# Performance work log

Hardware: AMD Instinct MI355X
Metric: run time of the kernel (lower is better)

## Reference

```python
import jax, jax.numpy as jnp
import numpy as np

N_NODES = 50000
N_EDGES = 600000
IN_DIM = 128
HID = 256
OUT = 3


def setup_inputs() -> dict:
    key = jax.random.key(0)
    ks = jax.random.split(key, 10)
    x = jax.random.normal(ks[0], (N_NODES, IN_DIM), dtype=jnp.float32)
    edge_index = jax.random.randint(ks[1], (2, N_EDGES), 0, N_NODES, dtype=jnp.int64)
    s = lambda k, shp: jax.random.normal(k, shp, dtype=jnp.float32) * (1.0 / np.sqrt(shp[0]))
    return {
        "x": x,
        "edge_index": edge_index,
        # SAGEConv1: lin_l (applied to aggregated neighbors, with bias), lin_r (root, no bias)
        "W1l": s(ks[2], (IN_DIM, HID)), "b1": jnp.zeros((HID,), jnp.float32), "W1r": s(ks[3], (IN_DIM, HID)),
        # SAGEConv2
        "W2l": s(ks[4], (HID, HID)), "b2": jnp.zeros((HID,), jnp.float32), "W2r": s(ks[5], (HID, HID)),
        # classification head
        "Wh": s(ks[6], (HID, OUT)), "bh": jnp.zeros((OUT,), jnp.float32),
    }


def _sage_conv(x, edge_index, Wl, b, Wr):
    """PyG SAGEConv with mean aggregation: out = lin_l(mean_{j->i} x_j) + lin_r(x_i)."""
    src, dst = edge_index[0], edge_index[1]
    n = x.shape[0]
    # gather source features and scatter-mean onto targets
    msg_sum = jax.ops.segment_sum(x[src], dst, num_segments=n)          # [N, d]
    deg = jax.ops.segment_sum(jnp.ones((src.shape[0],), x.dtype), dst, num_segments=n)
    mean = msg_sum / jnp.maximum(deg, 1.0)[:, None]                      # isolated nodes -> 0
    return mean @ Wl + b + x @ Wr


def reference(x, edge_index, W1l, b1, W1r, W2l, b2, W2r, Wh, bh):
    h = jax.nn.relu(_sage_conv(x, edge_index, W1l, b1, W1r))
    # dropout(p=0.2) is identity in eval mode
    h = jax.nn.relu(_sage_conv(h, edge_index, W2l, b2, W2r))
    return h @ Wh + bh
```

## Files before the change

### kernel.cpp

```cpp
#include <hip/hip_runtime.h>
#include <hip/hip_bf16.h>

#define N_NODES 50000
#define N_EDGES 600000
#define IN_DIM 128
#define HID 256
#define OUT_DIM 3

#define M_PAD 50048

#define SCAN_B 256
#define SCAN_NB ((N_NODES + SCAN_B - 1) / SCAN_B)

typedef __bf16 bf16x8 __attribute__((ext_vector_type(8)));
typedef float f32x4 __attribute__((ext_vector_type(4)));

static __device__ __forceinline__ unsigned short f2b(float f) {
    union { float f; unsigned u; } u; u.f = f;
    unsigned r = u.u + 0x7fffu + ((u.u >> 16) & 1u);
    return (unsigned short)(r >> 16);
}
static __device__ __forceinline__ float b2f(unsigned short b) {
    union { unsigned u; float f; } u; u.u = ((unsigned)b) << 16;
    return u.f;
}

static __device__ __forceinline__ void gload16(const void* g, unsigned short* l) {
    __builtin_amdgcn_global_load_lds((const __attribute__((address_space(1))) void*)g,
                                     (__attribute__((address_space(3))) void*)l, 16, 0, 0);
}


__global__ void count_deg_kernel(const int* __restrict__ dst, int* __restrict__ counts) {
    int e = blockIdx.x * blockDim.x + threadIdx.x;
    if (e < N_EDGES) atomicAdd(&counts[dst[e]], 1);
}

__global__ __launch_bounds__(256) void block_sum_kernel(const int* __restrict__ counts,
                                                        int* __restrict__ partial) {
    int node = blockIdx.x * SCAN_B + threadIdx.x;
    int v = (node < N_NODES) ? counts[node] : 0;
#pragma unroll
    for (int off = 32; off > 0; off >>= 1) v += __shfl_down(v, off);
    __shared__ int ws[4];
    if ((threadIdx.x & 63) == 0) ws[threadIdx.x >> 6] = v;
    __syncthreads();
    if (threadIdx.x == 0) partial[blockIdx.x] = ws[0] + ws[1] + ws[2] + ws[3];
}

__global__ __launch_bounds__(256) void scan_partial_kernel(int* __restrict__ partial) {
    __shared__ int s[SCAN_B];
    int t = threadIdx.x;
    int v = (t < SCAN_NB) ? partial[t] : 0;
    s[t] = v;
    __syncthreads();
    for (int off = 1; off < SCAN_B; off <<= 1) {
        int u = (t >= off) ? s[t - off] : 0;
        __syncthreads();
        s[t] += u;
        __syncthreads();
    }
    if (t < SCAN_NB) partial[t] = s[t] - v;
}

__global__ __launch_bounds__(256) void write_rowptr_kernel(const int* __restrict__ counts,
                                                           const int* __restrict__ partial,
                                                           int* __restrict__ row_ptr) {
    __shared__ int s[SCAN_B];
    int t = threadIdx.x;
    int node = blockIdx.x * SCAN_B + t;
    int v = (node < N_NODES) ? counts[node] : 0;
    s[t] = v;
    __syncthreads();
    for (int off = 1; off < SCAN_B; off <<= 1) {
        int u = (t >= off) ? s[t - off] : 0;
        __syncthreads();
        s[t] += u;
        __syncthreads();
    }
    if (node < N_NODES) row_ptr[node] = partial[blockIdx.x] + s[t] - v;
    if (node == 0) row_ptr[N_NODES] = N_EDGES;
}

__global__ void fill_csr_kernel(const int* __restrict__ src, const int* __restrict__ dst,
                                const int* __restrict__ row_ptr, int* __restrict__ cursor,
                                int* __restrict__ csr_src) {
    int e = blockIdx.x * blockDim.x + threadIdx.x;
    if (e < N_EDGES) {
        int d = dst[e];
        int pos = atomicAdd(&cursor[d], 1);
        csr_src[row_ptr[d] + pos] = src[e];
    }
}


__global__ void cast_f2b_kernel(const float* __restrict__ in, unsigned short* __restrict__ out, int n) {
    int i = blockIdx.x * blockDim.x + threadIdx.x;
    if (i * 4 < n) {
        float4 v = ((const float4*)in)[i];
        ushort4 o;
        o.x = f2b(v.x); o.y = f2b(v.y); o.z = f2b(v.z); o.w = f2b(v.w);
        ((ushort4*)out)[i] = o;
    }
}

__global__ void tcast4_kernel(const float* __restrict__ W1l, const float* __restrict__ W1r,
                              const float* __restrict__ W2l, const float* __restrict__ W2r,
                              unsigned short* __restrict__ W1lt, unsigned short* __restrict__ W1rt,
                              unsigned short* __restrict__ W2lt, unsigned short* __restrict__ W2rt) {
    int i = blockIdx.x * blockDim.x + threadIdx.x;
    const float* in; unsigned short* out; int K, base;
    if (i < 32768)        { in = W1l; out = W1lt; K = IN_DIM; base = 0; }
    else if (i < 65536)   { in = W1r; out = W1rt; K = IN_DIM; base = 32768; }
    else if (i < 131072)  { in = W2l; out = W2lt; K = HID;    base = 65536; }
    else if (i < 196608)  { in = W2r; out = W2rt; K = HID;    base = 131072; }
    else return;
    int j = i - base;
    int k = j >> 8;
    int n = j & 255;
    out[(size_t)n * K + k] = f2b(in[j]);
}

__global__ void init_out_kernel(const float* __restrict__ bh, float* __restrict__ out) {
    int i = blockIdx.x * blockDim.x + threadIdx.x;
    if (i < N_NODES * 3) out[i] = bh[i % 3];
}


static __device__ __forceinline__ void addv(float* acc, uint4 v) {
    acc[0] += b2f((unsigned short)(v.x & 0xffff));
    acc[1] += b2f((unsigned short)(v.x >> 16));
    acc[2] += b2f((unsigned short)(v.y & 0xffff));
    acc[3] += b2f((unsigned short)(v.y >> 16));
    acc[4] += b2f((unsigned short)(v.z & 0xffff));
    acc[5] += b2f((unsigned short)(v.z >> 16));
    acc[6] += b2f((unsigned short)(v.w & 0xffff));
    acc[7] += b2f((unsigned short)(v.w >> 16));
}

static __device__ __forceinline__ uint4 pack8(const float* a) {
    uint4 pk;
    pk.x = (unsigned)f2b(a[0]) | ((unsigned)f2b(a[1]) << 16);
    pk.y = (unsigned)f2b(a[2]) | ((unsigned)f2b(a[3]) << 16);
    pk.z = (unsigned)f2b(a[4]) | ((unsigned)f2b(a[5]) << 16);
    pk.w = (unsigned)f2b(a[6]) | ((unsigned)f2b(a[7]) << 16);
    return pk;
}

__global__ __launch_bounds__(256) void agg_mean256_kernel(const unsigned short* __restrict__ feat,
                                                          const int* __restrict__ row_ptr,
                                                          const int* __restrict__ csr_src,
                                                          unsigned short* __restrict__ out) {
    int node = blockIdx.x * 4 + (threadIdx.x >> 6);
    if (node >= N_NODES) return;
    int lane = threadIdx.x & 63;
    int half = lane >> 5, lh = lane & 31;
    const uint4* f4 = (const uint4*)feat;
    float acc[8];
#pragma unroll
    for (int j = 0; j < 8; j++) acc[j] = 0.f;
    int beg = row_ptr[node], end = row_ptr[node + 1];
    int i = beg;
    for (; i + 4 <= end; i += 4) {
        int sA = csr_src[i + half];
        int sB = csr_src[i + 2 + half];
        uint4 vA = f4[(size_t)sA * 32 + lh];
        uint4 vB = f4[(size_t)sB * 32 + lh];
        addv(acc, vA);
        addv(acc, vB);
    }
    if (i + 2 <= end) {
        int s = csr_src[i + half];
        addv(acc, f4[(size_t)s * 32 + lh]);
        i += 2;
    }
    if (i < end && half == 0) {
        int s = csr_src[i];
        addv(acc, f4[(size_t)s * 32 + lh]);
    }
    float inv = (end > beg) ? 1.0f / (float)(end - beg) : 0.0f;
#pragma unroll
    for (int j = 0; j < 8; j++) {
        acc[j] += __shfl_xor(acc[j], 32);
        acc[j] *= inv;
    }
    if (half == 0) ((uint4*)(out + (size_t)node * 256))[lh] = pack8(acc);
}

__global__ __launch_bounds__(256) void agg_mean128_kernel(const unsigned short* __restrict__ feat,
                                                          const int* __restrict__ row_ptr,
                                                          const int* __restrict__ csr_src,
                                                          unsigned short* __restrict__ out) {
    int node = blockIdx.x * 4 + (threadIdx.x >> 6);
    if (node >= N_NODES) return;
    int lane = threadIdx.x & 63;
    int q = lane >> 4, lq = lane & 15;
    const uint4* f4 = (const uint4*)feat;
    float acc[8];
#pragma unroll
    for (int j = 0; j < 8; j++) acc[j] = 0.f;
    int beg = row_ptr[node], end = row_ptr[node + 1];
    int i = beg;
    for (; i + 8 <= end; i += 8) {
        int sA = csr_src[i + q];
        int sB = csr_src[i + 4 + q];
        uint4 vA = f4[(size_t)sA * 16 + lq];
        uint4 vB = f4[(size_t)sB * 16 + lq];
        addv(acc, vA);
        addv(acc, vB);
    }
    if (i + 4 <= end) {
        int s = csr_src[i + q];
        addv(acc, f4[(size_t)s * 16 + lq]);
        i += 4;
    }
    int rem = end - i;
    if (q < rem) {
        int s = csr_src[i + q];
        addv(acc, f4[(size_t)s * 16 + lq]);
    }
    float inv = (end > beg) ? 1.0f / (float)(end - beg) : 0.0f;
#pragma unroll
    for (int j = 0; j < 8; j++) {
        acc[j] += __shfl_xor(acc[j], 32);
        acc[j] += __shfl_xor(acc[j], 16);
        acc[j] *= inv;
    }
    if (q == 0) ((uint4*)(out + (size_t)node * 128))[lq] = pack8(acc);
}


#define GEMM_STAGE_AND_MFMA(A, Wt)                                                          \
    for (int k0 = 0; k0 < K; k0 += 64) {                                                    \
        __syncthreads();                                                                    \
        _Pragma("unroll")                                                                   \
        for (int r = 0; r < 4; r++) {                                                       \
            int kb = skb + 2 * r;                                                           \
            gload16(A + (size_t)(m0 + sm) * K + k0 + kb * 8, &As[kb * 1024 + sm * 8]);      \
            gload16(Wt + (size_t)(n0 + sm) * K + k0 + kb * 8, &Bs[kb * 1024 + sm * 8]);     \
        }                                                                                   \
        __syncthreads();                                                                    \
        _Pragma("unroll")                                                                   \
        for (int kk = 0; kk < 2; kk++) {                                                    \
            int kbb = kk * 4 + quad;                                                        \
            bf16x8 a[2], b[8];                                                              \
            a[0] = *(const bf16x8*)&As[kbb * 1024 + (w * 32 + lr) * 8];                     \
            a[1] = *(const bf16x8*)&As[kbb * 1024 + (w * 32 + 16 + lr) * 8];                \
            _Pragma("unroll")                                                               \
            for (int nt = 0; nt < 8; nt++)                                                  \
                b[nt] = *(const bf16x8*)&Bs[kbb * 1024 + (nt * 16 + lr) * 8];               \
            _Pragma("unroll")                                                               \
            for (int mt = 0; mt < 2; mt++)                                                  \
                _Pragma("unroll")                                                           \
                for (int nt = 0; nt < 8; nt++)                                              \
                    acc[mt][nt] = __builtin_amdgcn_mfma_f32_16x16x32_bf16(a[mt], b[nt],     \
                                                                          acc[mt][nt], 0, 0, 0); \
        }                                                                                   \
    }

__global__ __launch_bounds__(256) void gemm_mfma_kernel(
    const unsigned short* __restrict__ A0, const unsigned short* __restrict__ W0t,
    const unsigned short* __restrict__ A1, const unsigned short* __restrict__ W1t,
    const float* __restrict__ bias, unsigned short* __restrict__ out,
    int M, int K) {
    __shared__ __align__(16) unsigned short As[8 * 128 * 8];
    __shared__ __align__(16) unsigned short Bs[8 * 128 * 8];

    const int t = threadIdx.x;
    const int w = t >> 6, l = t & 63;
    const int quad = l >> 4, lr = l & 15;
    const int m0 = blockIdx.x * 128, n0 = blockIdx.y * 128;
    const int sm = t & 127, skb = t >> 7;

    f32x4 acc[2][8];
    const f32x4 zero = {0.f, 0.f, 0.f, 0.f};
#pragma unroll
    for (int mt = 0; mt < 2; mt++)
#pragma unroll
        for (int nt = 0; nt < 8; nt++) acc[mt][nt] = zero;

    float bias_r[8];
#pragma unroll
    for (int nt = 0; nt < 8; nt++) bias_r[nt] = bias[n0 + nt * 16 + lr];

    GEMM_STAGE_AND_MFMA(A0, W0t)
    GEMM_STAGE_AND_MFMA(A1, W1t)

#pragma unroll
    for (int mt = 0; mt < 2; mt++)
#pragma unroll
        for (int r = 0; r < 4; r++) {
            int gm = m0 + w * 32 + mt * 16 + quad * 4 + r;
            if (gm >= M) continue;
            unsigned short* orow = out + (size_t)gm * HID;
#pragma unroll
            for (int nt = 0; nt < 8; nt++) {
                float v = fmaxf(acc[mt][nt][r] + bias_r[nt], 0.f);
                orow[n0 + nt * 16 + lr] = f2b(v);
            }
        }
}

__global__ __launch_bounds__(256) void gemm_mfma_head_kernel(
    const unsigned short* __restrict__ A0, const unsigned short* __restrict__ W0t,
    const unsigned short* __restrict__ A1, const unsigned short* __restrict__ W1t,
    const float* __restrict__ bias, const float* __restrict__ Wh,
    float* __restrict__ out, int M, int K) {
    __shared__ __align__(16) unsigned short As[8 * 128 * 8];
    __shared__ __align__(16) unsigned short Bs[8 * 128 * 8];

    const int t = threadIdx.x;
    const int w = t >> 6, l = t & 63;
    const int quad = l >> 4, lr = l & 15;
    const int m0 = blockIdx.x * 128, n0 = blockIdx.y * 128;
    const int sm = t & 127, skb = t >> 7;

    f32x4 acc[2][8];
    const f32x4 zero = {0.f, 0.f, 0.f, 0.f};
#pragma unroll
    for (int mt = 0; mt < 2; mt++)
#pragma unroll
        for (int nt = 0; nt < 8; nt++) acc[mt][nt] = zero;

    float bias_r[8];
    float wh_r[8][3];
#pragma unroll
    for (int nt = 0; nt < 8; nt++) {
        int gn = n0 + nt * 16 + lr;
        bias_r[nt] = bias[gn];
        wh_r[nt][0] = Wh[gn * 3 + 0];
        wh_r[nt][1] = Wh[gn * 3 + 1];
        wh_r[nt][2] = Wh[gn * 3 + 2];
    }

    GEMM_STAGE_AND_MFMA(A0, W0t)
    GEMM_STAGE_AND_MFMA(A1, W1t)

#pragma unroll
    for (int mt = 0; mt < 2; mt++)
#pragma unroll
        for (int r = 0; r < 4; r++) {
            int gm = m0 + w * 32 + mt * 16 + quad * 4 + r;
            float p0 = 0.f, p1 = 0.f, p2 = 0.f;
#pragma unroll
            for (int nt = 0; nt < 8; nt++) {
                float v = fmaxf(acc[mt][nt][r] + bias_r[nt], 0.f);
                p0 += v * wh_r[nt][0];
                p1 += v * wh_r[nt][1];
                p2 += v * wh_r[nt][2];
            }
#pragma unroll
            for (int off = 1; off < 16; off <<= 1) {
                p0 += __shfl_xor(p0, off);
                p1 += __shfl_xor(p1, off);
                p2 += __shfl_xor(p2, off);
            }
            if (lr == 0 && gm < M) {
                atomicAdd(&out[(size_t)gm * 3 + 0], p0);
                atomicAdd(&out[(size_t)gm * 3 + 1], p1);
                atomicAdd(&out[(size_t)gm * 3 + 2], p2);
            }
        }
}


extern "C" void kernel_launch(void* const* d_in, const int* in_sizes, int n_in,
                              void* d_out, int out_size, void* d_ws, size_t ws_size,
                              hipStream_t stream) {
    const float* x   = (const float*)d_in[0];
    const int*   ei  = (const int*)d_in[1];
    const int*   src = ei;
    const int*   dst = ei + N_EDGES;
    const float* W1l = (const float*)d_in[2];
    const float* b1  = (const float*)d_in[3];
    const float* W1r = (const float*)d_in[4];
    const float* W2l = (const float*)d_in[5];
    const float* b2  = (const float*)d_in[6];
    const float* W2r = (const float*)d_in[7];
    const float* Wh  = (const float*)d_in[8];
    const float* bh  = (const float*)d_in[9];
    float* out = (float*)d_out;

    char* ws = (char*)d_ws;
    size_t off = 0;
    auto alloc = [&](size_t bytes) -> void* {
        void* p = ws + off;
        off = (off + bytes + 255) & ~(size_t)255;
        return p;
    };
    int* counts   = (int*)alloc((size_t)N_NODES * 4);
    int* row_ptr  = (int*)alloc((size_t)(N_NODES + 1) * 4);
    int* cursor   = (int*)alloc((size_t)N_NODES * 4);
    int* partial  = (int*)alloc((size_t)SCAN_NB * 4);
    int* csr_src  = (int*)alloc((size_t)N_EDGES * 4);
    unsigned short* xb   = (unsigned short*)alloc((size_t)M_PAD * IN_DIM * 2);
    unsigned short* agg  = (unsigned short*)alloc((size_t)M_PAD * HID * 2);
    unsigned short* h1   = (unsigned short*)alloc((size_t)M_PAD * HID * 2);
    unsigned short* W1lt = (unsigned short*)alloc((size_t)IN_DIM * HID * 2);
    unsigned short* W1rt = (unsigned short*)alloc((size_t)IN_DIM * HID * 2);
    unsigned short* W2lt = (unsigned short*)alloc((size_t)HID * HID * 2);
    unsigned short* W2rt = (unsigned short*)alloc((size_t)HID * HID * 2);

    hipMemsetAsync(counts, 0, (size_t)N_NODES * 4, stream);
    hipMemsetAsync(cursor, 0, (size_t)N_NODES * 4, stream);

    const int eblocks = (N_EDGES + 255) / 256;
    count_deg_kernel<<<eblocks, 256, 0, stream>>>(dst, counts);
    block_sum_kernel<<<SCAN_NB, SCAN_B, 0, stream>>>(counts, partial);
    scan_partial_kernel<<<1, SCAN_B, 0, stream>>>(partial);
    write_rowptr_kernel<<<SCAN_NB, SCAN_B, 0, stream>>>(counts, partial, row_ptr);
    fill_csr_kernel<<<eblocks, 256, 0, stream>>>(src, dst, row_ptr, cursor, csr_src);

    {
        int n = N_NODES * IN_DIM;
        cast_f2b_kernel<<<(n / 4 + 255) / 256, 256, 0, stream>>>(x, xb, n);
        tcast4_kernel<<<(196608 + 255) / 256, 256, 0, stream>>>(W1l, W1r, W2l, W2r,
                                                                W1lt, W1rt, W2lt, W2rt);
        init_out_kernel<<<(N_NODES * 3 + 255) / 256, 256, 0, stream>>>(bh, out);
    }

    const int nblocks4 = (N_NODES + 3) / 4;
    dim3 gg((N_NODES + 127) / 128, HID / 128);

    agg_mean128_kernel<<<nblocks4, 256, 0, stream>>>(xb, row_ptr, csr_src, agg);
    gemm_mfma_kernel<<<gg, 256, 0, stream>>>(agg, W1lt, xb, W1rt, b1, h1, N_NODES, IN_DIM);

    agg_mean256_kernel<<<nblocks4, 256, 0, stream>>>(h1, row_ptr, csr_src, agg);
    gemm_mfma_head_kernel<<<gg, 256, 0, stream>>>(agg, W2lt, h1, W2rt, b2, Wh, out, N_NODES, HID);
}
```

Baseline: 307.9 us.

## Replace LDS-staged GEMM with direct register-loaded MFMA waves and narrower N tiles

Drops the shared-memory staging (global_load_lds plus barriers) in both GEMM kernels. Each wave now loads its A and W fragments straight from global memory into registers and feeds MFMA, with K as a template parameter so the loop fully unrolls. The N tile shrinks from 128 to 64 and the grid doubles in y, with a 4-blocks-per-SM occupancy hint. This removes LDS traffic and barrier stalls, but A rows are reused across fewer N columns and fragments are fetched repeatedly from global memory, which depends on the caches absorbing the duplication.

```diff
diff --git a/kernel.cpp b/kernel.cpp
--- a/kernel.cpp
+++ b/kernel.cpp
@@ -23,11 +23,6 @@
 static __device__ __forceinline__ float b2f(unsigned short b) {
     union { unsigned u; float f; } u; u.u = ((unsigned)b) << 16;
     return u.f;
-}
-
-static __device__ __forceinline__ void gload16(const void* g, unsigned short* l) {
-    __builtin_amdgcn_global_load_lds((const __attribute__((address_space(1))) void*)g,
-                                     (__attribute__((address_space(3))) void*)l, 16, 0, 0);
 }
 
 
@@ -230,102 +225,92 @@
 }
 
 
-#define GEMM_STAGE_AND_MFMA(A, Wt)                                                          \
-    for (int k0 = 0; k0 < K; k0 += 64) {                                                    \
-        __syncthreads();                                                                    \
-        _Pragma("unroll")                                                                   \
-        for (int r = 0; r < 4; r++) {                                                       \
-            int kb = skb + 2 * r;                                                           \
-            gload16(A + (size_t)(m0 + sm) * K + k0 + kb * 8, &As[kb * 1024 + sm * 8]);      \
-            gload16(Wt + (size_t)(n0 + sm) * K + k0 + kb * 8, &Bs[kb * 1024 + sm * 8]);     \
-        }                                                                                   \
-        __syncthreads();                                                                    \
-        _Pragma("unroll")                                                                   \
-        for (int kk = 0; kk < 2; kk++) {                                                    \
-            int kbb = kk * 4 + quad;                                                        \
-            bf16x8 a[2], b[8];                                                              \
-            a[0] = *(const bf16x8*)&As[kbb * 1024 + (w * 32 + lr) * 8];                     \
-            a[1] = *(const bf16x8*)&As[kbb * 1024 + (w * 32 + 16 + lr) * 8];                \
-            _Pragma("unroll")                                                               \
-            for (int nt = 0; nt < 8; nt++)                                                  \
-                b[nt] = *(const bf16x8*)&Bs[kbb * 1024 + (nt * 16 + lr) * 8];               \
-            _Pragma("unroll")                                                               \
-            for (int mt = 0; mt < 2; mt++)                                                  \
-                _Pragma("unroll")                                                           \
-                for (int nt = 0; nt < 8; nt++)                                              \
-                    acc[mt][nt] = __builtin_amdgcn_mfma_f32_16x16x32_bf16(a[mt], b[nt],     \
-                                                                          acc[mt][nt], 0, 0, 0); \
-        }                                                                                   \
-    }
-
-__global__ __launch_bounds__(256) void gemm_mfma_kernel(
+template <int K>
+static __device__ __forceinline__ void gemm_wave(const unsigned short* __restrict__ A,
+                                                 const unsigned short* __restrict__ Wt,
+                                                 int arow, int n0, int lr, int quad,
+                                                 f32x4 (&acc)[2][4]) {
+#pragma unroll
+    for (int ks = 0; ks < K / 32; ks++) {
+        const int koff = ks * 32 + quad * 8;
+        bf16x8 a[2], b[4];
+#pragma unroll
+        for (int mt = 0; mt < 2; mt++)
+            a[mt] = *(const bf16x8*)(A + (size_t)(arow + mt * 16 + lr) * K + koff);
+#pragma unroll
+        for (int nt = 0; nt < 4; nt++)
+            b[nt] = *(const bf16x8*)(Wt + (size_t)(n0 + nt * 16 + lr) * K + koff);
+#pragma unroll
+        for (int mt = 0; mt < 2; mt++)
+#pragma unroll
+            for (int nt = 0; nt < 4; nt++)
+                acc[mt][nt] = __builtin_amdgcn_mfma_f32_16x16x32_bf16(a[mt], b[nt], acc[mt][nt], 0, 0, 0);
+    }
+}
+
+template <int K>
+__global__ __launch_bounds__(256, 4) void gemm_reg_kernel(
     const unsigned short* __restrict__ A0, const unsigned short* __restrict__ W0t,
     const unsigned short* __restrict__ A1, const unsigned short* __restrict__ W1t,
-    const float* __restrict__ bias, unsigned short* __restrict__ out,
-    int M, int K) {
-    __shared__ __align__(16) unsigned short As[8 * 128 * 8];
-    __shared__ __align__(16) unsigned short Bs[8 * 128 * 8];
-
+    const float* __restrict__ bias, unsigned short* __restrict__ out, int M) {
     const int t = threadIdx.x;
     const int w = t >> 6, l = t & 63;
     const int quad = l >> 4, lr = l & 15;
-    const int m0 = blockIdx.x * 128, n0 = blockIdx.y * 128;
-    const int sm = t & 127, skb = t >> 7;
-
-    f32x4 acc[2][8];
+    const int arow = blockIdx.x * 128 + w * 32;
+    const int n0 = blockIdx.y * 64;
+
+    f32x4 acc[2][4];
     const f32x4 zero = {0.f, 0.f, 0.f, 0.f};
 #pragma unroll
     for (int mt = 0; mt < 2; mt++)
 #pragma unroll
-        for (int nt = 0; nt < 8; nt++) acc[mt][nt] = zero;
-
-    float bias_r[8];
-#pragma unroll
-    for (int nt = 0; nt < 8; nt++) bias_r[nt] = bias[n0 + nt * 16 + lr];
-
-    GEMM_STAGE_AND_MFMA(A0, W0t)
-    GEMM_STAGE_AND_MFMA(A1, W1t)
+        for (int nt = 0; nt < 4; nt++) acc[mt][nt] = zero;
+
+    float bias_r[4];
+#pragma unroll
+    for (int nt = 0; nt < 4; nt++) bias_r[nt] = bias[n0 + nt * 16 + lr];
+
+    gemm_wave<K>(A0, W0t, arow, n0, lr, quad, acc);
+    gemm_wave<K>(A1, W1t, arow, n0, lr, quad, acc);
 
 #pragma unroll
     for (int mt = 0; mt < 2; mt++)
 #pragma unroll
         for (int r = 0; r < 4; r++) {
-            int gm = m0 + w * 32 + mt * 16 + quad * 4 + r;
+            int gm = arow + mt * 16 + quad * 4 + r;
             if (gm >= M) continue;
             unsigned short* orow = out + (size_t)gm * HID;
 #pragma unroll
-            for (int nt = 0; nt < 8; nt++) {
+            for (int nt = 0; nt < 4; nt++) {
                 float v = fmaxf(acc[mt][nt][r] + bias_r[nt], 0.f);
                 orow[n0 + nt * 16 + lr] = f2b(v);
             }
         }
 }
 
-__global__ __launch_bounds__(256) void gemm_mfma_head_kernel(
+template <int K>
+__global__ __launch_bounds__(256, 4) void gemm_reg_head_kernel(
     const unsigned short* __restrict__ A0, const unsigned short* __restrict__ W0t,
     const unsigned short* __restrict__ A1, const unsigned short* __restrict__ W1t,
     const float* __restrict__ bias, const float* __restrict__ Wh,
-    float* __restrict__ out, int M, int K) {
-    __shared__ __align__(16) unsigned short As[8 * 128 * 8];
-    __shared__ __align__(16) unsigned short Bs[8 * 128 * 8];
-
+    float* __restrict__ out, int M) {
     const int t = threadIdx.x;
     const int w = t >> 6, l = t & 63;
     const int quad = l >> 4, lr = l & 15;
-    const int m0 = blockIdx.x * 128, n0 = blockIdx.y * 128;
-    const int sm = t & 127, skb = t >> 7;
-
-    f32x4 acc[2][8];
+    const int arow = blockIdx.x * 128 + w * 32;
+    const int n0 = blockIdx.y * 64;
+
+    f32x4 acc[2][4];
     const f32x4 zero = {0.f, 0.f, 0.f, 0.f};
 #pragma unroll
     for (int mt = 0; mt < 2; mt++)
 #pragma unroll
-        for (int nt = 0; nt < 8; nt++) acc[mt][nt] = zero;
-
-    float bias_r[8];
-    float wh_r[8][3];
-#pragma unroll
-    for (int nt = 0; nt < 8; nt++) {
+        for (int nt = 0; nt < 4; nt++) acc[mt][nt] = zero;
+
+    float bias_r[4];
+    float wh_r[4][3];
+#pragma unroll
+    for (int nt = 0; nt < 4; nt++) {
         int gn = n0 + nt * 16 + lr;
         bias_r[nt] = bias[gn];
         wh_r[nt][0] = Wh[gn * 3 + 0];
@@ -333,17 +318,17 @@
         wh_r[nt][2] = Wh[gn * 3 + 2];
     }
 
-    GEMM_STAGE_AND_MFMA(A0, W0t)
-    GEMM_STAGE_AND_MFMA(A1, W1t)
+    gemm_wave<K>(A0, W0t, arow, n0, lr, quad, acc);
+    gemm_wave<K>(A1, W1t, arow, n0, lr, quad, acc);
 
 #pragma unroll
     for (int mt = 0; mt < 2; mt++)
 #pragma unroll
         for (int r = 0; r < 4; r++) {
-            int gm = m0 + w * 32 + mt * 16 + quad * 4 + r;
+            int gm = arow + mt * 16 + quad * 4 + r;
             float p0 = 0.f, p1 = 0.f, p2 = 0.f;
 #pragma unroll
-            for (int nt = 0; nt < 8; nt++) {
+            for (int nt = 0; nt < 4; nt++) {
                 float v = fmaxf(acc[mt][nt][r] + bias_r[nt], 0.f);
                 p0 += v * wh_r[nt][0];
                 p1 += v * wh_r[nt][1];
@@ -420,11 +405,11 @@
     }
 
     const int nblocks4 = (N_NODES + 3) / 4;
-    dim3 gg((N_NODES + 127) / 128, HID / 128);
+    dim3 gg((N_NODES + 127) / 128, HID / 64);
 
     agg_mean128_kernel<<<nblocks4, 256, 0, stream>>>(xb, row_ptr, csr_src, agg);
-    gemm_mfma_kernel<<<gg, 256, 0, stream>>>(agg, W1lt, xb, W1rt, b1, h1, N_NODES, IN_DIM);
+    gemm_reg_kernel<IN_DIM><<<gg, 256, 0, stream>>>(agg, W1lt, xb, W1rt, b1, h1, N_NODES);
 
     agg_mean256_kernel<<<nblocks4, 256, 0, stream>>>(h1, row_ptr, csr_src, agg);
-    gemm_mfma_head_kernel<<<gg, 256, 0, stream>>>(agg, W2lt, h1, W2rt, b2, Wh, out, N_NODES, HID);
-}
+    gemm_reg_head_kernel<HID><<<gg, 256, 0, stream>>>(agg, W2lt, h1, W2rt, b2, Wh, out, N_NODES);
+}
```

Result: slower. 352.2 us (+14.4%).

## Double-buffer GEMM tiles with register prefetch instead of direct LDS loads

Applied to the files above, without the earlier changes.

Replaces the single-buffer global_load_lds staging in both fused SAGE GEMM kernels with a register-prefetched, double-buffered LDS pipeline over K chunks of 32. The next tile's global loads are issued before the MFMAs on the current buffer, so memory latency can overlap compute and one barrier per iteration is dropped. The K chunk shrinks from 64 to 32, so there are more iterations, and staging through registers adds VGPR pressure and extra LDS write instructions.

```diff
diff --git a/kernel.cpp b/kernel.cpp
--- a/kernel.cpp
+++ b/kernel.cpp
@@ -23,11 +23,6 @@
 static __device__ __forceinline__ float b2f(unsigned short b) {
     union { unsigned u; float f; } u; u.u = ((unsigned)b) << 16;
     return u.f;
-}
-
-static __device__ __forceinline__ void gload16(const void* g, unsigned short* l) {
-    __builtin_amdgcn_global_load_lds((const __attribute__((address_space(1))) void*)g,
-                                     (__attribute__((address_space(3))) void*)l, 16, 0, 0);
 }
 
 
@@ -230,47 +225,77 @@
 }
 
 
-#define GEMM_STAGE_AND_MFMA(A, Wt)                                                          \
-    for (int k0 = 0; k0 < K; k0 += 64) {                                                    \
-        __syncthreads();                                                                    \
-        _Pragma("unroll")                                                                   \
-        for (int r = 0; r < 4; r++) {                                                       \
-            int kb = skb + 2 * r;                                                           \
-            gload16(A + (size_t)(m0 + sm) * K + k0 + kb * 8, &As[kb * 1024 + sm * 8]);      \
-            gload16(Wt + (size_t)(n0 + sm) * K + k0 + kb * 8, &Bs[kb * 1024 + sm * 8]);     \
-        }                                                                                   \
-        __syncthreads();                                                                    \
-        _Pragma("unroll")                                                                   \
-        for (int kk = 0; kk < 2; kk++) {                                                    \
-            int kbb = kk * 4 + quad;                                                        \
-            bf16x8 a[2], b[8];                                                              \
-            a[0] = *(const bf16x8*)&As[kbb * 1024 + (w * 32 + lr) * 8];                     \
-            a[1] = *(const bf16x8*)&As[kbb * 1024 + (w * 32 + 16 + lr) * 8];                \
-            _Pragma("unroll")                                                               \
-            for (int nt = 0; nt < 8; nt++)                                                  \
-                b[nt] = *(const bf16x8*)&Bs[kbb * 1024 + (nt * 16 + lr) * 8];               \
-            _Pragma("unroll")                                                               \
-            for (int mt = 0; mt < 2; mt++)                                                  \
-                _Pragma("unroll")                                                           \
-                for (int nt = 0; nt < 8; nt++)                                              \
-                    acc[mt][nt] = __builtin_amdgcn_mfma_f32_16x16x32_bf16(a[mt], b[nt],     \
-                                                                          acc[mt][nt], 0, 0, 0); \
-        }                                                                                   \
-    }
-
-__global__ __launch_bounds__(256) void gemm_mfma_kernel(
+template <int KP>
+static __device__ __forceinline__ void gemm_pipe_loop(
     const unsigned short* __restrict__ A0, const unsigned short* __restrict__ W0t,
     const unsigned short* __restrict__ A1, const unsigned short* __restrict__ W1t,
-    const float* __restrict__ bias, unsigned short* __restrict__ out,
-    int M, int K) {
-    __shared__ __align__(16) unsigned short As[8 * 128 * 8];
-    __shared__ __align__(16) unsigned short Bs[8 * 128 * 8];
+    unsigned short* As, unsigned short* Bs,
+    int m0, int n0, int t, int w, int quad, int lr, f32x4 (&acc)[2][8]) {
+    constexpr int KI = KP / 32;
+    constexpr int NIT = 2 * KI;
+    const int kb = t & 3;
+    const int r  = t >> 2;
+
+    const unsigned short* Aa[2] = {A0, A1};
+    const unsigned short* Wa[2] = {W0t, W1t};
+
+    uint4 ra0, ra1, rb0, rb1;
+    auto gload = [&](int it) {
+        int p = it / KI;
+        int k0 = (it % KI) * 32 + kb * 8;
+        const unsigned short* A = Aa[p];
+        const unsigned short* Wt = Wa[p];
+        ra0 = *(const uint4*)(A + (size_t)(m0 + r) * KP + k0);
+        ra1 = *(const uint4*)(A + (size_t)(m0 + 64 + r) * KP + k0);
+        rb0 = *(const uint4*)(Wt + (size_t)(n0 + r) * KP + k0);
+        rb1 = *(const uint4*)(Wt + (size_t)(n0 + 64 + r) * KP + k0);
+    };
+    auto wlds = [&](int buf) {
+        unsigned short* pa = As + buf * 4096;
+        unsigned short* pb = Bs + buf * 4096;
+        *(uint4*)&pa[(kb * 128 + r) * 8] = ra0;
+        *(uint4*)&pa[(kb * 128 + 64 + r) * 8] = ra1;
+        *(uint4*)&pb[(kb * 128 + r) * 8] = rb0;
+        *(uint4*)&pb[(kb * 128 + 64 + r) * 8] = rb1;
+    };
+
+    gload(0);
+    wlds(0);
+    __syncthreads();
+    for (int it = 0; it < NIT; ++it) {
+        if (it + 1 < NIT) gload(it + 1);
+        const unsigned short* pa = As + (it & 1) * 4096;
+        const unsigned short* pb = Bs + (it & 1) * 4096;
+        bf16x8 a[2], b[8];
+        a[0] = *(const bf16x8*)&pa[(quad * 128 + w * 32 + lr) * 8];
+        a[1] = *(const bf16x8*)&pa[(quad * 128 + w * 32 + 16 + lr) * 8];
+#pragma unroll
+        for (int nt = 0; nt < 8; nt++)
+            b[nt] = *(const bf16x8*)&pb[(quad * 128 + nt * 16 + lr) * 8];
+#pragma unroll
+        for (int mt = 0; mt < 2; mt++)
+#pragma unroll
+            for (int nt = 0; nt < 8; nt++)
+                acc[mt][nt] = __builtin_amdgcn_mfma_f32_16x16x32_bf16(a[mt], b[nt], acc[mt][nt], 0, 0, 0);
+        if (it + 1 < NIT) {
+            wlds((it + 1) & 1);
+            __syncthreads();
+        }
+    }
+}
+
+template <int KP>
+__global__ __launch_bounds__(256) void gemm_pipe_kernel(
+    const unsigned short* __restrict__ A0, const unsigned short* __restrict__ W0t,
+    const unsigned short* __restrict__ A1, const unsigned short* __restrict__ W1t,
+    const float* __restrict__ bias, unsigned short* __restrict__ out, int M) {
+    __shared__ __align__(16) unsigned short As[2 * 4096];
+    __shared__ __align__(16) unsigned short Bs[2 * 4096];
 
     const int t = threadIdx.x;
     const int w = t >> 6, l = t & 63;
     const int quad = l >> 4, lr = l & 15;
     const int m0 = blockIdx.x * 128, n0 = blockIdx.y * 128;
-    const int sm = t & 127, skb = t >> 7;
 
     f32x4 acc[2][8];
     const f32x4 zero = {0.f, 0.f, 0.f, 0.f};
@@ -283,8 +308,7 @@
 #pragma unroll
     for (int nt = 0; nt < 8; nt++) bias_r[nt] = bias[n0 + nt * 16 + lr];
 
-    GEMM_STAGE_AND_MFMA(A0, W0t)
-    GEMM_STAGE_AND_MFMA(A1, W1t)
+    gemm_pipe_loop<KP>(A0, W0t, A1, W1t, As, Bs, m0, n0, t, w, quad, lr, acc);
 
 #pragma unroll
     for (int mt = 0; mt < 2; mt++)
@@ -301,19 +325,19 @@
         }
 }
 
-__global__ __launch_bounds__(256) void gemm_mfma_head_kernel(
+template <int KP>
+__global__ __launch_bounds__(256) void gemm_pipe_head_kernel(
     const unsigned short* __restrict__ A0, const unsigned short* __restrict__ W0t,
     const unsigned short* __restrict__ A1, const unsigned short* __restrict__ W1t,
     const float* __restrict__ bias, const float* __restrict__ Wh,
-    float* __restrict__ out, int M, int K) {
-    __shared__ __align__(16) unsigned short As[8 * 128 * 8];
-    __shared__ __align__(16) unsigned short Bs[8 * 128 * 8];
+    float* __restrict__ out, int M) {
+    __shared__ __align__(16) unsigned short As[2 * 4096];
+    __shared__ __align__(16) unsigned short Bs[2 * 4096];
 
     const int t = threadIdx.x;
     const int w = t >> 6, l = t & 63;
     const int quad = l >> 4, lr = l & 15;
     const int m0 = blockIdx.x * 128, n0 = blockIdx.y * 128;
-    const int sm = t & 127, skb = t >> 7;
 
     f32x4 acc[2][8];
     const f32x4 zero = {0.f, 0.f, 0.f, 0.f};
@@ -333,8 +357,7 @@
         wh_r[nt][2] = Wh[gn * 3 + 2];
     }
 
-    GEMM_STAGE_AND_MFMA(A0, W0t)
-    GEMM_STAGE_AND_MFMA(A1, W1t)
+    gemm_pipe_loop<KP>(A0, W0t, A1, W1t, As, Bs, m0, n0, t, w, quad, lr, acc);
 
 #pragma unroll
     for (int mt = 0; mt < 2; mt++)
@@ -420,11 +443,11 @@
     }
 
     const int nblocks4 = (N_NODES + 3) / 4;
-    dim3 gg((N_NODES + 127) / 128, HID / 128);
+    dim3 gg(M_PAD / 128, HID / 128);
 
     agg_mean128_kernel<<<nblocks4, 256, 0, stream>>>(xb, row_ptr, csr_src, agg);
-    gemm_mfma_kernel<<<gg, 256, 0, stream>>>(agg, W1lt, xb, W1rt, b1, h1, N_NODES, IN_DIM);
+    gemm_pipe_kernel<IN_DIM><<<gg, 256, 0, stream>>>(agg, W1lt, xb, W1rt, b1, h1, N_NODES);
 
     agg_mean256_kernel<<<nblocks4, 256, 0, stream>>>(h1, row_ptr, csr_src, agg);
-    gemm_mfma_head_kernel<<<gg, 256, 0, stream>>>(agg, W2lt, h1, W2rt, b2, Wh, out, N_NODES, HID);
-}
+    gemm_pipe_head_kernel<HID><<<gg, 256, 0, stream>>>(agg, W2lt, h1, W2rt, b2, Wh, out, N_NODES);
+}
```

Result: faster. 289.8 us (-5.9%).
